# Optimization experiments

Measured on AMD Instinct MI355X. Metric: run time of the kernel, lower is better.

The kernel has to match this reference:

```python
import jax, jax.numpy as jnp
import numpy as np

NUM_ITERATIONS = 4
STEP = 1
N_NODES = 50000
N_EDGES = 800000
D_FEAT = 64


def setup_inputs() -> dict:
    key = jax.random.key(0)
    k1, k2, k3 = jax.random.split(key, 3)
    x = jax.random.normal(k1, (N_NODES, D_FEAT), dtype=jnp.float32)
    src = jax.random.randint(k2, (N_EDGES,), 0, N_NODES, dtype=jnp.int64)
    dst = jax.random.randint(k3, (N_EDGES,), 0, N_NODES, dtype=jnp.int64)
    edge_index = jnp.stack([src, dst], axis=0)
    return {"x": x, "edge_index": edge_index}


def _wl_conv(x, src, dst, n_nodes):
    # continuous WL: x_i' = 0.5 * (x_i + mean_{j in N(i)} x_j)
    msg = x[src]  # [E, D] gather of neighbor features
    summed = jax.ops.segment_sum(msg, dst, num_segments=n_nodes)  # [N, D]
    deg = jax.ops.segment_sum(jnp.ones_like(dst, dtype=x.dtype), dst,
                              num_segments=n_nodes)  # [N]
    mean = summed / jnp.maximum(deg, 1.0)[:, None]  # isolated nodes -> 0
    return 0.5 * (x + mean)


def reference(x, edge_index):
    n_nodes = x.shape[0]
    src, dst = edge_index[0], edge_index[1]
    feats = [x]
    for _ in range(NUM_ITERATIONS):
        for _ in range(STEP):
            x = _wl_conv(x, src, dst, n_nodes)
        feats.append(x)
    return jnp.concatenate(feats, axis=-1)  # [N, (num_iterations+1)*D]
```

## Files before the change

kernel.cpp:

```cpp
#include <hip/hip_runtime.h>

constexpr int N = 50000;
constexpr int E = 800000;
constexpr int D = 64;
constexpr int DOUT = 320;
constexpr int CAPD = 64;
constexpr int NBUCK = (N + 255) / 256;
constexpr int SLAB = 5120;
constexpr int PART_BLOCKS = 256;
constexpr int CONV_BLOCKS = (N * 16 + 255) / 256;
constexpr int ITER_BLOCKS = 2048;
constexpr int SCAN_BLOCKS = (N + 255) / 256;

__device__ __forceinline__ unsigned short f2bf(float f) {
    unsigned int u = __float_as_uint(f);
    unsigned int r = (u + 0x7fffu + ((u >> 16) & 1u)) >> 16;
    return (unsigned short)r;
}
__device__ __forceinline__ unsigned int pack2(float a, float b) {
    return (unsigned int)f2bf(a) | ((unsigned int)f2bf(b) << 16);
}
__device__ __forceinline__ float bflo(unsigned int u) { return __uint_as_float(u << 16); }
__device__ __forceinline__ float bfhi(unsigned int u) { return __uint_as_float(u & 0xFFFF0000u); }

__global__ __launch_bounds__(256) void part_conv_kernel(
    const int* __restrict__ ei32,
    const float* __restrict__ x,
    float* __restrict__ out,
    unsigned int* __restrict__ mirror,
    int* __restrict__ cursor,
    unsigned int* __restrict__ slab) {
    if (blockIdx.x >= PART_BLOCKS) {
        int i = (blockIdx.x - PART_BLOCKS) * 256 + threadIdx.x;
        if (i < N * 16) {
            int n = i >> 4, j = i & 15;
            float4 v = ((const float4*)x)[i];
            ((float4*)(out + (size_t)n * DOUT))[j] = v;
            uint2 m = make_uint2(pack2(v.x, v.y), pack2(v.z, v.w));
            ((uint2*)(mirror + (size_t)n * 32))[j] = m;
        }
        return;
    }
    __shared__ int hcnt[NBUCK];
    __shared__ int hbase[NBUCK];
    int t = threadIdx.x;
    for (int k = t; k < NBUCK; k += 256) hcnt[k] = 0;
    int lane = t & 63;
    int wv = ei32[2 * lane + 1];
    int is64 = (__ballot(wv != 0) == 0ULL) ? 1 : 0;
    __syncthreads();

    const int EPB = E / PART_BLOCKS;
    int i0 = blockIdx.x * EPB;
    for (int k = t; k < EPB; k += 256) {
        int i = i0 + k;
        int d = is64 ? ei32[2 * (E + i)] : ei32[E + i];
        atomicAdd(&hcnt[d >> 8], 1);
    }
    __syncthreads();
    for (int k = t; k < NBUCK; k += 256) {
        hbase[k] = atomicAdd(&cursor[k], hcnt[k]);
        hcnt[k] = 0;
    }
    __syncthreads();
    for (int k = t; k < EPB; k += 256) {
        int i = i0 + k;
        int s = is64 ? ei32[2 * i] : ei32[i];
        int d = is64 ? ei32[2 * (E + i)] : ei32[E + i];
        int b = d >> 8;
        int r = atomicAdd(&hcnt[b], 1);
        int p = hbase[b] + r;
        if (p < SLAB)
            slab[(size_t)b * SLAB + p] = (unsigned int)s | ((unsigned int)(d & 255) << 16);
    }
}

__global__ __launch_bounds__(256) void lds_build_kernel(
    const unsigned int* __restrict__ slab,
    const int* __restrict__ cursor,
    int* __restrict__ cnt,
    unsigned short* __restrict__ csr) {
    __shared__ unsigned short rows[256 * CAPD];
    __shared__ int lcnt[256];
    int b = blockIdx.x;
    int t = threadIdx.x;
    lcnt[t] = 0;
    __syncthreads();
    int sz = min(cursor[b], SLAB);
    const unsigned int* sp = slab + (size_t)b * SLAB;
    for (int k = t; k < sz; k += 256) {
        unsigned int rec = sp[k];
        int dlo = (rec >> 16) & 255;
        int r = atomicAdd(&lcnt[dlo], 1);
        if (r < CAPD) rows[dlo * CAPD + r] = (unsigned short)(rec & 0xFFFFu);
    }
    __syncthreads();
    int node = b * 256 + t;
    if (node < N) cnt[node] = min(lcnt[t], CAPD);
    for (int k = t; k < 256 * (CAPD / 8); k += 256) {
        int nd = k >> 3;
        int j = k & 7;
        int g = b * 256 + nd;
        if (g < N && j * 8 < lcnt[nd]) {
            *(uint4*)(csr + (size_t)g * CAPD + j * 8) =
                *(const uint4*)(rows + nd * CAPD + j * 8);
        }
    }
}


__global__ __launch_bounds__(256) void wl_iter_bf16_kernel(
    const unsigned int* __restrict__ min_,
    unsigned int* __restrict__ mout,
    const float* __restrict__ self_in,
    float* __restrict__ xout,
    const int* __restrict__ cnt, const unsigned short* __restrict__ csr) {
    int gw = blockIdx.x * 4 + (threadIdx.x >> 6);
    int lane = threadIdx.x & 63;
    int g = lane >> 3;
    int fi = lane & 7;
    const int NW = ITER_BLOCKS * 4;

    int deg_cur = (gw < N) ? min(cnt[gw], CAPD) : 0;
    for (int w = gw; w < N; w += NW) {
        int wn = w + NW;
        int deg_nxt = (wn < N) ? min(cnt[wn], CAPD) : 0;
        int deg = deg_cur;
        size_t base = (size_t)w * CAPD;

        float a[8], b[8];
#pragma unroll
        for (int k = 0; k < 8; ++k) { a[k] = 0.f; b[k] = 0.f; }

#define ACC8(u, arr)                                                     \
        arr[0] += bflo(u.x); arr[1] += bfhi(u.x);                        \
        arr[2] += bflo(u.y); arr[3] += bfhi(u.y);                        \
        arr[4] += bflo(u.z); arr[5] += bfhi(u.z);                        \
        arr[6] += bflo(u.w); arr[7] += bfhi(u.w);

        int e = g;
        for (; e + 8 < deg; e += 16) {
            int s0 = csr[base + e], s1 = csr[base + e + 8];
            uint4 u0 = *(const uint4*)(min_ + (size_t)s0 * 32 + fi * 4);
            uint4 u1 = *(const uint4*)(min_ + (size_t)s1 * 32 + fi * 4);
            ACC8(u0, a); ACC8(u1, b);
        }
        if (e < deg) {
            int s = csr[base + e];
            uint4 u = *(const uint4*)(min_ + (size_t)s * 32 + fi * 4);
            ACC8(u, a);
        }
#undef ACC8
#pragma unroll
        for (int k = 0; k < 8; ++k) {
            a[k] += b[k];
            a[k] += __shfl_xor(a[k], 8);
            a[k] += __shfl_xor(a[k], 16);
            a[k] += __shfl_xor(a[k], 32);
        }
        float inv = (deg > 0) ? 0.5f / (float)deg : 0.0f;
        if (g == 0) {
            const float* srow = self_in + (size_t)w * DOUT + fi * 8;
            float4 s0 = *(const float4*)(srow);
            float4 s1 = *(const float4*)(srow + 4);
            float r0 = 0.5f * s0.x + inv * a[0];
            float r1 = 0.5f * s0.y + inv * a[1];
            float r2 = 0.5f * s0.z + inv * a[2];
            float r3 = 0.5f * s0.w + inv * a[3];
            float r4 = 0.5f * s1.x + inv * a[4];
            float r5 = 0.5f * s1.y + inv * a[5];
            float r6 = 0.5f * s1.z + inv * a[6];
            float r7 = 0.5f * s1.w + inv * a[7];
            float* drow = xout + (size_t)w * DOUT + fi * 8;
            *(float4*)(drow)     = make_float4(r0, r1, r2, r3);
            *(float4*)(drow + 4) = make_float4(r4, r5, r6, r7);
            if (mout) {
                uint4 m = make_uint4(pack2(r0, r1), pack2(r2, r3),
                                     pack2(r4, r5), pack2(r6, r7));
                *(uint4*)(mout + (size_t)w * 32 + fi * 4) = m;
            }
        }
        deg_cur = deg_nxt;
    }
}


__global__ void detect_kernel(const int* __restrict__ ei32, int* __restrict__ flag) {
    if (blockIdx.x == 0 && threadIdx.x == 0) {
        int s = 0;
        for (int k = 0; k < 128; ++k) s |= ei32[2 * k + 1];
        *flag = (s == 0) ? 1 : 0;
    }
}
__device__ __forceinline__ int load_src(const int* ei32, int is64, int i) {
    return is64 ? ei32[2 * i] : ei32[i];
}
__device__ __forceinline__ int load_dst(const int* ei32, int is64, int i) {
    return is64 ? ei32[2 * (E + i)] : ei32[E + i];
}

__global__ __launch_bounds__(256) void hist_kernel(const int* __restrict__ ei32,
                                                   const int* __restrict__ flag,
                                                   int* __restrict__ cnt) {
    int i = blockIdx.x * 256 + threadIdx.x;
    int is64 = *flag;
    if (i < E) atomicAdd(&cnt[load_dst(ei32, is64, i)], 1);
}

__global__ __launch_bounds__(256) void scan1_kernel(const int* __restrict__ cnt,
                                                    int* __restrict__ offs,
                                                    int* __restrict__ P) {
    __shared__ int sm[256];
    int t = threadIdx.x;
    int i = blockIdx.x * 256 + t;
    int v = (i < N) ? cnt[i] : 0;
    sm[t] = v; __syncthreads();
    for (int o = 1; o < 256; o <<= 1) {
        int u = (t >= o) ? sm[t - o] : 0;
        __syncthreads();
        sm[t] += u;
        __syncthreads();
    }
    if (i < N) offs[i] = sm[t] - v;
    if (t == 255) P[blockIdx.x] = sm[255];
}

__global__ __launch_bounds__(256) void scan2_kernel(int* __restrict__ P,
                                                    int* __restrict__ offs) {
    __shared__ int sm[256];
    int t = threadIdx.x;
    int v = (t < SCAN_BLOCKS) ? P[t] : 0;
    sm[t] = v; __syncthreads();
    for (int o = 1; o < 256; o <<= 1) {
        int u = (t >= o) ? sm[t - o] : 0;
        __syncthreads();
        sm[t] += u;
        __syncthreads();
    }
    if (t < SCAN_BLOCKS) P[t] = sm[t] - v;
    if (t == 255) offs[N] = sm[255];
}

__global__ __launch_bounds__(256) void scan3_kernel(int* __restrict__ offs,
                                                    const int* __restrict__ P) {
    int i = blockIdx.x * 256 + threadIdx.x;
    if (i < N) offs[i] += P[blockIdx.x];
}

__global__ __launch_bounds__(256) void scatter_kernel(const int* __restrict__ ei32,
                                                      const int* __restrict__ flag,
                                                      const int* __restrict__ offs,
                                                      int* __restrict__ cursor,
                                                      int* __restrict__ csr) {
    int i = blockIdx.x * 256 + threadIdx.x;
    int is64 = *flag;
    if (i < E) {
        int d = load_dst(ei32, is64, i);
        int p = atomicAdd(&cursor[d], 1);
        csr[offs[d] + p] = load_src(ei32, is64, i);
    }
}

__global__ __launch_bounds__(256) void chunk0_kernel(const float* __restrict__ x,
                                                     float* __restrict__ out) {
    int i = blockIdx.x * 256 + threadIdx.x;
    if (i < N * 16) {
        int n = i >> 4, j = i & 15;
        float4 v = ((const float4*)x)[i];
        ((float4*)(out + (size_t)n * DOUT))[j] = v;
    }
}

__global__ __launch_bounds__(256) void wl_iter_kernel(
    const float* __restrict__ xin, float* __restrict__ xout,
    const int* __restrict__ offs, const int* __restrict__ csr) {
    int w = blockIdx.x * 4 + (threadIdx.x >> 6);
    if (w >= N) return;
    int lane = threadIdx.x & 63;
    int g = lane >> 4, fi = lane & 15;
    int beg = offs[w], end = offs[w + 1];
    float4 a0 = make_float4(0.f, 0.f, 0.f, 0.f);
    float4 a1 = make_float4(0.f, 0.f, 0.f, 0.f);
    int e = beg + g;
    for (; e + 4 < end; e += 8) {
        int s0 = csr[e], s1 = csr[e + 4];
        float4 v0 = *(const float4*)(xin + (size_t)s0 * DOUT + fi * 4);
        float4 v1 = *(const float4*)(xin + (size_t)s1 * DOUT + fi * 4);
        a0.x += v0.x; a0.y += v0.y; a0.z += v0.z; a0.w += v0.w;
        a1.x += v1.x; a1.y += v1.y; a1.z += v1.z; a1.w += v1.w;
    }
    if (e < end) {
        int s = csr[e];
        float4 v = *(const float4*)(xin + (size_t)s * DOUT + fi * 4);
        a0.x += v.x; a0.y += v.y; a0.z += v.z; a0.w += v.w;
    }
    float4 acc;
    acc.x = a0.x + a1.x; acc.y = a0.y + a1.y;
    acc.z = a0.z + a1.z; acc.w = a0.w + a1.w;
    acc.x += __shfl_xor(acc.x, 16); acc.y += __shfl_xor(acc.y, 16);
    acc.z += __shfl_xor(acc.z, 16); acc.w += __shfl_xor(acc.w, 16);
    acc.x += __shfl_xor(acc.x, 32); acc.y += __shfl_xor(acc.y, 32);
    acc.z += __shfl_xor(acc.z, 32); acc.w += __shfl_xor(acc.w, 32);
    int deg = end - beg;
    float inv = (deg > 0) ? 0.5f / (float)deg : 0.0f;
    if (g == 0) {
        float4 s4 = *(const float4*)(xin + (size_t)w * DOUT + fi * 4);
        float4 r;
        r.x = 0.5f * s4.x + inv * acc.x;
        r.y = 0.5f * s4.y + inv * acc.y;
        r.z = 0.5f * s4.z + inv * acc.z;
        r.w = 0.5f * s4.w + inv * acc.w;
        *(float4*)(xout + (size_t)w * DOUT + fi * 4) = r;
    }
}


extern "C" void kernel_launch(void* const* d_in, const int* in_sizes, int n_in,
                              void* d_out, int out_size, void* d_ws, size_t ws_size,
                              hipStream_t stream) {
    const float* x  = (const float*)d_in[0];
    const int* ei32 = (const int*)d_in[1];
    float* out = (float*)d_out;

    int* cursor = (int*)d_ws;
    int* cnt = cursor + 256;
    unsigned int* slab = (unsigned int*)(cnt + N);
    unsigned short* csr = (unsigned short*)(slab + (size_t)NBUCK * SLAB);
    unsigned int* mirA = (unsigned int*)((char*)csr + (size_t)N * CAPD * 2);
    unsigned int* mirB = mirA + (size_t)N * 32;
    size_t need = 256 * 4 + (size_t)N * 4 + (size_t)NBUCK * SLAB * 4 +
                  (size_t)N * CAPD * 2 + (size_t)2 * N * 32 * 4;

    dim3 b256(256);
    dim3 gE((E + 255) / 256);
    dim3 gIter(ITER_BLOCKS);
    dim3 gConv((N * 16 + 255) / 256);

    if (ws_size >= need) {
        hipMemsetAsync(cursor, 0, 256 * sizeof(int), stream);
        part_conv_kernel<<<dim3(PART_BLOCKS + CONV_BLOCKS), b256, 0, stream>>>(
            ei32, x, out, mirA, cursor, slab);
        lds_build_kernel<<<dim3(NBUCK), b256, 0, stream>>>(slab, cursor, cnt, csr);
        wl_iter_bf16_kernel<<<gIter, b256, 0, stream>>>(
            mirA, mirB, out + 0 * D, out + 1 * D, cnt, csr);
        wl_iter_bf16_kernel<<<gIter, b256, 0, stream>>>(
            mirB, mirA, out + 1 * D, out + 2 * D, cnt, csr);
        wl_iter_bf16_kernel<<<gIter, b256, 0, stream>>>(
            mirA, mirB, out + 2 * D, out + 3 * D, cnt, csr);
        wl_iter_bf16_kernel<<<gIter, b256, 0, stream>>>(
            mirB, (unsigned int*)nullptr, out + 3 * D, out + 4 * D, cnt, csr);
    } else {
        int* flag  = (int*)d_ws;
        int* fcnt  = flag + 16;
        int* foffs = fcnt + N;
        int* P     = foffs + (N + 1);
        int* fcsr  = P + 256;
        detect_kernel<<<1, 64, 0, stream>>>(ei32, flag);
        hipMemsetAsync(fcnt, 0, (size_t)N * 4, stream);
        hist_kernel<<<gE, b256, 0, stream>>>(ei32, flag, fcnt);
        scan1_kernel<<<dim3(SCAN_BLOCKS), b256, 0, stream>>>(fcnt, foffs, P);
        scan2_kernel<<<1, b256, 0, stream>>>(P, foffs);
        scan3_kernel<<<dim3(SCAN_BLOCKS), b256, 0, stream>>>(foffs, P);
        hipMemsetAsync(fcnt, 0, (size_t)N * 4, stream);
        scatter_kernel<<<gE, b256, 0, stream>>>(ei32, flag, foffs, fcnt, fcsr);
        chunk0_kernel<<<gConv, b256, 0, stream>>>(x, out);
        for (int c = 1; c <= 4; ++c) {
            wl_iter_kernel<<<dim3((N + 3) / 4), b256, 0, stream>>>(
                out + (size_t)(c - 1) * D, out + (size_t)c * D, foffs, fcsr);
        }
    }
}
```

Baseline: 204.1 us.

## Software-pipeline WL gather with sentinel-padded CSR and zero mirror row

Pads each CSR row up to a multiple of 16 (at least 32) with a sentinel index N that points at a zeroed extra row in both bf16 mirrors. The gather can then issue the first 32 neighbor loads unconditionally without per-edge bounds checks. The iteration kernel is restructured into a two-node software pipeline: it prefetches the CSR indices and degree for the node after next, and issues gathers for the next node while consuming the current one. This is meant to hide gather latency. Launch geometry also changes (more partition blocks, 512-thread CSR build, fewer iteration blocks with an occupancy hint), at the cost of higher register pressure and some wasted loads for low-degree nodes.

Result: slower. 370.4 us (+81.5%).

```diff
diff --git a/kernel.cpp b/kernel.cpp
--- a/kernel.cpp
+++ b/kernel.cpp
@@ -5,11 +5,12 @@
 constexpr int D = 64;
 constexpr int DOUT = 320;
 constexpr int CAPD = 64;
+constexpr int SENT = N;
 constexpr int NBUCK = (N + 255) / 256;
 constexpr int SLAB = 5120;
-constexpr int PART_BLOCKS = 256;
-constexpr int CONV_BLOCKS = (N * 16 + 255) / 256;
-constexpr int ITER_BLOCKS = 2048;
+constexpr int PART_BLOCKS = 400;
+constexpr int CONV_BLOCKS = ((N + 1) * 16 + 255) / 256;
+constexpr int ITER_BLOCKS = 1280;
 constexpr int SCAN_BLOCKS = (N + 255) / 256;
 
 __device__ __forceinline__ unsigned short f2bf(float f) {
@@ -27,17 +28,24 @@
     const int* __restrict__ ei32,
     const float* __restrict__ x,
     float* __restrict__ out,
-    unsigned int* __restrict__ mirror,
+    unsigned int* __restrict__ mirA,
+    unsigned int* __restrict__ mirB,
     int* __restrict__ cursor,
     unsigned int* __restrict__ slab) {
     if (blockIdx.x >= PART_BLOCKS) {
         int i = (blockIdx.x - PART_BLOCKS) * 256 + threadIdx.x;
-        if (i < N * 16) {
+        if (i < (N + 1) * 16) {
             int n = i >> 4, j = i & 15;
-            float4 v = ((const float4*)x)[i];
-            ((float4*)(out + (size_t)n * DOUT))[j] = v;
-            uint2 m = make_uint2(pack2(v.x, v.y), pack2(v.z, v.w));
-            ((uint2*)(mirror + (size_t)n * 32))[j] = m;
+            if (n < N) {
+                float4 v = ((const float4*)x)[i];
+                ((float4*)(out + (size_t)n * DOUT))[j] = v;
+                uint2 m = make_uint2(pack2(v.x, v.y), pack2(v.z, v.w));
+                ((uint2*)(mirA + (size_t)n * 32))[j] = m;
+            } else {
+                uint2 z = make_uint2(0u, 0u);
+                ((uint2*)(mirA + (size_t)N * 32))[j] = z;
+                ((uint2*)(mirB + (size_t)N * 32))[j] = z;
+            }
         }
         return;
     }
@@ -75,7 +83,7 @@
     }
 }
 
-__global__ __launch_bounds__(256) void lds_build_kernel(
+__global__ __launch_bounds__(512) void lds_build_kernel(
     const unsigned int* __restrict__ slab,
     const int* __restrict__ cursor,
     int* __restrict__ cnt,
@@ -84,11 +92,13 @@
     __shared__ int lcnt[256];
     int b = blockIdx.x;
     int t = threadIdx.x;
-    lcnt[t] = 0;
+    if (t < 256) lcnt[t] = 0;
+    unsigned int* rw = (unsigned int*)rows;
+    for (int k = t; k < 256 * CAPD / 2; k += 512) rw[k] = 0xC350C350u;
     __syncthreads();
     int sz = min(cursor[b], SLAB);
     const unsigned int* sp = slab + (size_t)b * SLAB;
-    for (int k = t; k < sz; k += 256) {
+    for (int k = t; k < sz; k += 512) {
         unsigned int rec = sp[k];
         int dlo = (rec >> 16) & 255;
         int r = atomicAdd(&lcnt[dlo], 1);
@@ -96,12 +106,13 @@
     }
     __syncthreads();
     int node = b * 256 + t;
-    if (node < N) cnt[node] = min(lcnt[t], CAPD);
-    for (int k = t; k < 256 * (CAPD / 8); k += 256) {
+    if (t < 256 && node < N) cnt[node] = min(lcnt[t], CAPD);
+    for (int k = t; k < 256 * (CAPD / 8); k += 512) {
         int nd = k >> 3;
         int j = k & 7;
         int g = b * 256 + nd;
-        if (g < N && j * 8 < lcnt[nd]) {
+        int padded = min(CAPD, max(32, (lcnt[nd] + 15) & ~15));
+        if (g < N && j * 8 < padded) {
             *(uint4*)(csr + (size_t)g * CAPD + j * 8) =
                 *(const uint4*)(rows + nd * CAPD + j * 8);
         }
@@ -109,80 +120,122 @@
 }
 
 
-__global__ __launch_bounds__(256) void wl_iter_bf16_kernel(
+#define ACC8(u, arr)                                                     \
+        arr[0] += bflo(u.x); arr[1] += bfhi(u.x);                        \
+        arr[2] += bflo(u.y); arr[3] += bfhi(u.y);                        \
+        arr[4] += bflo(u.z); arr[5] += bfhi(u.z);                        \
+        arr[6] += bflo(u.w); arr[7] += bfhi(u.w);
+
+__global__ __launch_bounds__(256, 5) void wl_iter_bf16_kernel(
     const unsigned int* __restrict__ min_,
     unsigned int* __restrict__ mout,
     const float* __restrict__ self_in,
     float* __restrict__ xout,
     const int* __restrict__ cnt, const unsigned short* __restrict__ csr) {
+    const int NW = ITER_BLOCKS * 4;
     int gw = blockIdx.x * 4 + (threadIdx.x >> 6);
     int lane = threadIdx.x & 63;
     int g = lane >> 3;
     int fi = lane & 7;
-    const int NW = ITER_BLOCKS * 4;
-
-    int deg_cur = (gw < N) ? min(cnt[gw], CAPD) : 0;
-    for (int w = gw; w < N; w += NW) {
-        int wn = w + NW;
-        int deg_nxt = (wn < N) ? min(cnt[wn], CAPD) : 0;
-        int deg = deg_cur;
-        size_t base = (size_t)w * CAPD;
-
-        float a[8], b[8];
+
+    uint4 Z = make_uint4(0u, 0u, 0u, 0u);
+
+#define GATHER(s) (*(const uint4*)(min_ + (size_t)(s) * 32 + fi * 4))
+
+    auto prefetch_csr = [&](int wx, int& cv, int& p0, int& p1, int& p2, int& p3) {
+        size_t bx = (size_t)wx * CAPD;
+        cv = cnt[wx];
+        p0 = (int)csr[bx + g];
+        p1 = (int)csr[bx + g + 8];
+        p2 = (int)csr[bx + g + 16];
+        p3 = (int)csr[bx + g + 24];
+    };
+    auto issue = [&](int wx, int cv, int p0, int p1, int p2, int p3,
+                     int& degx, uint4& q0, uint4& q1, uint4& q2, uint4& q3,
+                     float4& sx0, float4& sx1) {
+        degx = min(cv, CAPD);
+        q0 = GATHER(p0);
+        q1 = GATHER(p1);
+        if (degx > 16) { q2 = GATHER(p2); q3 = GATHER(p3); }
+        if (g == 0) {
+            const float* sr = self_in + (size_t)wx * DOUT + fi * 8;
+            sx0 = *(const float4*)(sr);
+            sx1 = *(const float4*)(sr + 4);
+        }
+    };
+    auto consume = [&](int wx, int degx, uint4 q0, uint4 q1, uint4 q2, uint4 q3,
+                       float4 sx0, float4 sx1) {
+        float a[8];
 #pragma unroll
-        for (int k = 0; k < 8; ++k) { a[k] = 0.f; b[k] = 0.f; }
-
-#define ACC8(u, arr)                                                     \
-        arr[0] += bflo(u.x); arr[1] += bfhi(u.x);                        \
-        arr[2] += bflo(u.y); arr[3] += bfhi(u.y);                        \
-        arr[4] += bflo(u.z); arr[5] += bfhi(u.z);                        \
-        arr[6] += bflo(u.w); arr[7] += bfhi(u.w);
-
-        int e = g;
-        for (; e + 8 < deg; e += 16) {
-            int s0 = csr[base + e], s1 = csr[base + e + 8];
-            uint4 u0 = *(const uint4*)(min_ + (size_t)s0 * 32 + fi * 4);
-            uint4 u1 = *(const uint4*)(min_ + (size_t)s1 * 32 + fi * 4);
-            ACC8(u0, a); ACC8(u1, b);
-        }
-        if (e < deg) {
-            int s = csr[base + e];
-            uint4 u = *(const uint4*)(min_ + (size_t)s * 32 + fi * 4);
-            ACC8(u, a);
-        }
-#undef ACC8
+        for (int k = 0; k < 8; ++k) a[k] = 0.f;
+        ACC8(q0, a); ACC8(q1, a);
+        if (degx > 16) { ACC8(q2, a); ACC8(q3, a); }
+        if (degx > 32) {
+            size_t bx = (size_t)wx * CAPD;
+            int pd = (degx + 15) & ~15;
+            for (int e = 32; e < pd; e += 16) {
+                int x0 = (int)csr[bx + g + e];
+                int x1 = (int)csr[bx + g + e + 8];
+                uint4 y0 = GATHER(x0);
+                uint4 y1 = GATHER(x1);
+                ACC8(y0, a); ACC8(y1, a);
+            }
+        }
 #pragma unroll
         for (int k = 0; k < 8; ++k) {
-            a[k] += b[k];
             a[k] += __shfl_xor(a[k], 8);
             a[k] += __shfl_xor(a[k], 16);
             a[k] += __shfl_xor(a[k], 32);
         }
-        float inv = (deg > 0) ? 0.5f / (float)deg : 0.0f;
+        float inv = (degx > 0) ? 0.5f / (float)degx : 0.0f;
         if (g == 0) {
-            const float* srow = self_in + (size_t)w * DOUT + fi * 8;
-            float4 s0 = *(const float4*)(srow);
-            float4 s1 = *(const float4*)(srow + 4);
-            float r0 = 0.5f * s0.x + inv * a[0];
-            float r1 = 0.5f * s0.y + inv * a[1];
-            float r2 = 0.5f * s0.z + inv * a[2];
-            float r3 = 0.5f * s0.w + inv * a[3];
-            float r4 = 0.5f * s1.x + inv * a[4];
-            float r5 = 0.5f * s1.y + inv * a[5];
-            float r6 = 0.5f * s1.z + inv * a[6];
-            float r7 = 0.5f * s1.w + inv * a[7];
-            float* drow = xout + (size_t)w * DOUT + fi * 8;
-            *(float4*)(drow)     = make_float4(r0, r1, r2, r3);
-            *(float4*)(drow + 4) = make_float4(r4, r5, r6, r7);
+            float o0 = 0.5f * sx0.x + inv * a[0];
+            float o1 = 0.5f * sx0.y + inv * a[1];
+            float o2 = 0.5f * sx0.z + inv * a[2];
+            float o3 = 0.5f * sx0.w + inv * a[3];
+            float o4 = 0.5f * sx1.x + inv * a[4];
+            float o5 = 0.5f * sx1.y + inv * a[5];
+            float o6 = 0.5f * sx1.z + inv * a[6];
+            float o7 = 0.5f * sx1.w + inv * a[7];
+            float* dr = xout + (size_t)wx * DOUT + fi * 8;
+            *(float4*)(dr)     = make_float4(o0, o1, o2, o3);
+            *(float4*)(dr + 4) = make_float4(o4, o5, o6, o7);
             if (mout) {
-                uint4 m = make_uint4(pack2(r0, r1), pack2(r2, r3),
-                                     pack2(r4, r5), pack2(r6, r7));
-                *(uint4*)(mout + (size_t)w * 32 + fi * 4) = m;
+                uint4 m = make_uint4(pack2(o0, o1), pack2(o2, o3),
+                                     pack2(o4, o5), pack2(o6, o7));
+                *(uint4*)(mout + (size_t)wx * 32 + fi * 4) = m;
             }
         }
-        deg_cur = deg_nxt;
-    }
-}
+    };
+
+    int w0 = gw;
+    int cvA, a0, a1, a2, a3;
+    prefetch_csr(w0, cvA, a0, a1, a2, a3);
+    int degA; uint4 uA0 = Z, uA1 = Z, uA2 = Z, uA3 = Z; float4 sA0, sA1;
+    issue(w0, cvA, a0, a1, a2, a3, degA, uA0, uA1, uA2, uA3, sA0, sA1);
+    int w1 = w0 + NW;
+    bool hB = (w1 < N);
+    int cvB = 0, b0 = 0, b1 = 0, b2 = 0, b3 = 0;
+    int degB; uint4 uB0 = Z, uB1 = Z, uB2 = Z, uB3 = Z; float4 sB0, sB1;
+    if (hB) prefetch_csr(w1, cvB, b0, b1, b2, b3);
+
+    while (true) {
+        if (hB) issue(w1, cvB, b0, b1, b2, b3, degB, uB0, uB1, uB2, uB3, sB0, sB1);
+        int w2 = w0 + 2 * NW;
+        if (w2 < N) prefetch_csr(w2, cvA, a0, a1, a2, a3);
+        consume(w0, degA, uA0, uA1, uA2, uA3, sA0, sA1);
+        if (!hB) break;
+        bool hA2 = (w2 < N);
+        if (hA2) issue(w2, cvA, a0, a1, a2, a3, degA, uA0, uA1, uA2, uA3, sA0, sA1);
+        int w3 = w1 + 2 * NW;
+        if (w3 < N) prefetch_csr(w3, cvB, b0, b1, b2, b3);
+        consume(w1, degB, uB0, uB1, uB2, uB3, sB0, sB1);
+        if (!hA2) break;
+        w0 = w2; w1 = w3; hB = (w3 < N);
+    }
+#undef GATHER
+}
+#undef ACC8
 
 
 __global__ void detect_kernel(const int* __restrict__ ei32, int* __restrict__ flag) {
@@ -327,9 +380,9 @@
     unsigned int* slab = (unsigned int*)(cnt + N);
     unsigned short* csr = (unsigned short*)(slab + (size_t)NBUCK * SLAB);
     unsigned int* mirA = (unsigned int*)((char*)csr + (size_t)N * CAPD * 2);
-    unsigned int* mirB = mirA + (size_t)N * 32;
+    unsigned int* mirB = mirA + (size_t)(N + 1) * 32;
     size_t need = 256 * 4 + (size_t)N * 4 + (size_t)NBUCK * SLAB * 4 +
-                  (size_t)N * CAPD * 2 + (size_t)2 * N * 32 * 4;
+                  (size_t)N * CAPD * 2 + (size_t)2 * (N + 1) * 32 * 4;
 
     dim3 b256(256);
     dim3 gE((E + 255) / 256);
@@ -339,8 +392,8 @@
     if (ws_size >= need) {
         hipMemsetAsync(cursor, 0, 256 * sizeof(int), stream);
         part_conv_kernel<<<dim3(PART_BLOCKS + CONV_BLOCKS), b256, 0, stream>>>(
-            ei32, x, out, mirA, cursor, slab);
-        lds_build_kernel<<<dim3(NBUCK), b256, 0, stream>>>(slab, cursor, cnt, csr);
+            ei32, x, out, mirA, mirB, cursor, slab);
+        lds_build_kernel<<<dim3(NBUCK), dim3(512), 0, stream>>>(slab, cursor, cnt, csr);
         wl_iter_bf16_kernel<<<gIter, b256, 0, stream>>>(
             mirA, mirB, out + 0 * D, out + 1 * D, cnt, csr);
         wl_iter_bf16_kernel<<<gIter, b256, 0, stream>>>(
```
